# Optimization experiments

Measured on AMD Instinct MI355X. Metric: run time of the kernel, lower is better.

The kernel has to match this reference:

```python
import jax, jax.numpy as jnp
import numpy as np

K = 3
N_SENSOR = 10   # num_sensor N (forced by reshape(-1,10,10))
ADJ_N = 5       # adjacency size (forced by reshape(-1,5,5))
T_LEN = 4096    # seq_len
BATCH = 1024    # batch_size == num_of_filters (forced by output accumulation)


def _scaled_laplacian(W):
    # L_tilde = 2L/lambda_max - I, L = D - W (W symmetric -> eigvalsh valid)
    D = jnp.diag(jnp.sum(W, axis=1))
    L = D - W
    lam_max = jnp.max(jnp.linalg.eigvalsh(L))
    return (2.0 * L) / lam_max - jnp.eye(W.shape[0], dtype=W.dtype)


def _cheb_polynomials(L_tilde, K):
    polys = [jnp.eye(L_tilde.shape[0], dtype=L_tilde.dtype), L_tilde]
    for _ in range(2, K):
        polys.append(2.0 * (L_tilde @ polys[-1]) - polys[-2])
    return jnp.stack(polys[:K])  # (K, 5, 5)


def setup_inputs() -> dict:
    key = jax.random.key(0)
    kx, ka, ks, kt = jax.random.split(key, 4)
    x = jax.random.normal(kx, (T_LEN, BATCH, N_SENSOR), dtype=jnp.float32)
    W = jax.random.uniform(ka, (ADJ_N, ADJ_N), dtype=jnp.float32)
    # symmetric, zero-diagonal adjacency so the Laplacian is symmetric PSD-ish
    adj_mx = (W + W.T) * 0.5 * (1.0 - jnp.eye(ADJ_N, dtype=jnp.float32))
    spatial_attention = jax.random.uniform(ks, (BATCH, N_SENSOR, N_SENSOR), dtype=jnp.float32)
    Theta = jax.random.normal(kt, (K, N_SENSOR, BATCH), dtype=jnp.float32)  # (K, num_of_timesteps=10, num_of_filters=B)
    return {"x": x, "adj_mx": adj_mx, "spatial_attention": spatial_attention, "Theta": Theta}


def reference(x, adj_mx, spatial_attention, Theta):
    # adj path is detached in the torch code (cpu().detach().numpy())
    L_tilde = _scaled_laplacian(jax.lax.stop_gradient(adj_mx))
    cheb = _cheb_polynomials(L_tilde, K)                 # (K, 5, 5)
    T, B, N = x.shape                                    # (T, B, 10)
    x_t = jnp.swapaxes(x, 0, 2)                          # (10, B, T)
    sa = spatial_attention.reshape(-1, ADJ_N, ADJ_N)     # (4B, 5, 5)
    output = jnp.zeros((T, B, N), dtype=x.dtype)
    for k in range(K):
        T_k_with_at = (cheb[k] * sa).reshape(-1, N, N)   # (B, 10, 10)
        lhs = jnp.swapaxes(T_k_with_at, 0, 2)            # (10, 10, B)
        rhs = jnp.matmul(lhs, x_t)                       # (10, 10, B) @ (10, B, T) -> (10, 10, T)
        out_k = jnp.matmul(jnp.swapaxes(rhs, 1, 2), Theta[k])  # (10, T, 10) @ (10, B) -> (10, T, B)
        output = output + jnp.transpose(out_k, (1, 2, 0))       # (T, B, 10)
    return jax.nn.relu(output[..., None])                # (T, B, 10, 1)
```

## Files before the change

kernel.cpp:

```cpp
#include <hip/hip_runtime.h>
#include <math.h>

#define TLEN 4096
#define NB   1024
#define NS   10

typedef __attribute__((ext_vector_type(8))) short  s16x8;
typedef __attribute__((ext_vector_type(4))) float  f32x4;

__device__ void k0_body(const float* __restrict__ adj, float* __restrict__ ck) {
  float Wm[5][5], L[5][5];
  for (int r = 0; r < 5; ++r)
    for (int c = 0; c < 5; ++c) Wm[r][c] = adj[r*5+c];
  for (int r = 0; r < 5; ++r) {
    float d = 0.f;
    for (int c = 0; c < 5; ++c) d += Wm[r][c];
    for (int c = 0; c < 5; ++c) L[r][c] = (r==c ? d : 0.f) - Wm[r][c];
  }
  float v[5] = {0.7f, -1.1f, 0.9f, -0.8f, 1.3f};
  for (int it = 0; it < 96; ++it) {
    float w[5];
    for (int r = 0; r < 5; ++r) {
      float s = 0.f;
      for (int c = 0; c < 5; ++c) s += L[r][c]*v[c];
      w[r] = s;
    }
    float s = fabsf(w[0])+fabsf(w[1])+fabsf(w[2])+fabsf(w[3])+fabsf(w[4]);
    float inv = 1.f/s;
    for (int r = 0; r < 5; ++r) v[r] = w[r]*inv;
  }
  float num = 0.f, den = 0.f;
  for (int r = 0; r < 5; ++r) {
    float s = 0.f;
    for (int c = 0; c < 5; ++c) s += L[r][c]*v[c];
    num += v[r]*s; den += v[r]*v[r];
  }
  const float lam = num/den;
  float Lt[5][5];
  for (int r = 0; r < 5; ++r)
    for (int c = 0; c < 5; ++c)
      Lt[r][c] = 2.f*L[r][c]/lam - (r==c ? 1.f : 0.f);
  float T2[5][5];
  for (int r = 0; r < 5; ++r)
    for (int c = 0; c < 5; ++c) {
      float s = 0.f;
      for (int j = 0; j < 5; ++j) s += Lt[r][j]*Lt[j][c];
      T2[r][c] = 2.f*s - (r==c ? 1.f : 0.f);
    }
  for (int p = 0; p < 10; ++p)
    for (int n = 0; n < 10; ++n) {
      int m = (10*p+n) % 25, r = m/5, c = m%5;
      ck[0*100 + p*10+n] = (r==c ? 1.f : 0.f);
      ck[1*100 + p*10+n] = Lt[r][c];
      ck[2*100 + p*10+n] = T2[r][c];
    }
}

static __device__ __forceinline__ unsigned bfu(float f) {
  unsigned u = __float_as_uint(f);
  return (u + 0x7FFFu + ((u >> 16) & 1u)) >> 16;
}
static __device__ __forceinline__ unsigned pk2(float lo, float hi) {
  return bfu(lo) | (bfu(hi) << 16);
}

#define KC   128
#define NCHK 4
#define XB_U32 10240

__global__ __launch_bounds__(384) void ka_mfma(
    const float* __restrict__ x, const float* __restrict__ sa,
    const float* __restrict__ adj, float* __restrict__ ps,
    float* __restrict__ ck) {
  __shared__ __align__(16) unsigned lds[2*XB_U32];
  unsigned* XB = lds;
  unsigned* AS = lds + XB_U32;
  const int tid = threadIdx.x;
  if (tid >= 320) {
    if (tid == 320 && blockIdx.x == 0 && blockIdx.y == 0) k0_body(adj, ck);
    return;
  }
  const int w    = tid >> 6;
  const int l    = tid & 63;
  const int tl16 = l & 15;
  const int t0   = blockIdx.x * 16;
  const int b0   = blockIdx.y * 512;
  const int n0   = 2*w, n1 = 2*w + 1;

  const int xbp = tid / 5;
  const int xg  = (tid - xbp*5) * 2;
  const int xk  = 2*xbp;
  const int xks = xk >> 5, xkg = (xk & 31) >> 3, xj = xk & 7;
  const int xbase0 = ((xg*4 + xks)*64 + xkg*16)*4 + (xj >> 1);

  f32x4 acc0 = {0.f,0.f,0.f,0.f}, acc1 = {0.f,0.f,0.f,0.f};

  for (int c = 0; c < NCHK; ++c) {
    const int bc = b0 + c*KC;
    {
      const float* gp0 = x + (size_t)t0*(NB*NS) + (size_t)bc*NS + xbp*20 + xg;
      #pragma unroll
      for (int r = 0; r < 16; ++r) {
        const float* gp = gp0 + (size_t)r*(NB*NS);
        const float2 lo = *(const float2*)(gp);
        const float2 hi = *(const float2*)(gp + NS);
        const int base = xbase0 + r*4;
        XB[base]        = pk2(lo.x, hi.x);
        XB[base + 1024] = pk2(lo.y, hi.y);
      }
    }
    #pragma unroll
    for (int r = 0; r < 10; ++r) {
      const int s  = tid + 320*r;
      const int bp = s / 50;
      const int g  = (s - bp*50) * 2;
      const int p  = g / 10, n = g - p*10;
      const int k  = 2*bp;
      const float* gp = sa + (size_t)(bc + k)*100 + g;
      const float2 lo = *(const float2*)(gp);
      const float2 hi = *(const float2*)(gp + 100);
      const int ks = k >> 5, kg = (k & 31) >> 3, j = k & 7;
      const int base = ((n*4 + ks)*64 + kg*16 + p)*4 + (j >> 1);
      AS[base]        = pk2(lo.x, hi.x);
      AS[base + 1024] = pk2(lo.y, hi.y);
    }
    __syncthreads();
    const s16x8* XBf = (const s16x8*)XB;
    const s16x8* ASf = (const s16x8*)AS;
    #pragma unroll
    for (int ks = 0; ks < 4; ++ks) {
      const s16x8 a0 = ASf[(n0*4 + ks)*64 + l];
      const s16x8 bb0 = XBf[(n0*4 + ks)*64 + l];
      acc0 = __builtin_amdgcn_mfma_f32_16x16x32_bf16(a0, bb0, acc0, 0, 0, 0);
      const s16x8 a1 = ASf[(n1*4 + ks)*64 + l];
      const s16x8 bb1 = XBf[(n1*4 + ks)*64 + l];
      acc1 = __builtin_amdgcn_mfma_f32_16x16x32_bf16(a1, bb1, acc1, 0, 0, 0);
    }
    __syncthreads();
  }
  const int pg = (l >> 4) * 4;
  float* pd = ps + ((size_t)blockIdx.y*TLEN + t0 + tl16)*100;
  #pragma unroll
  for (int r = 0; r < 4; ++r) {
    const int p = pg + r;
    if (p < 10) {
      pd[n0*10 + p] = acc0[r];
      pd[n1*10 + p] = acc1[r];
    }
  }
}

#define TT 8
__global__ __launch_bounds__(256) void kc_out(const float* __restrict__ theta,
    const float* __restrict__ ck, const float* __restrict__ ps,
    float* __restrict__ out) {
  __shared__ __align__(16) float S[TT*120];
  __shared__ float C[300];
  __shared__ __align__(16) float stg[2][2560];
  const int tid = threadIdx.x;
  const int t0 = blockIdx.x * TT;
  const int b  = blockIdx.y * 256 + tid;
  for (int j = tid; j < 300; j += 256) C[j] = ck[j];
  for (int j = tid; j < TT*100; j += 256) {
    const int tt = j / 100, q = j - tt*100;
    float s = 0.f;
    #pragma unroll
    for (int sl = 0; sl < 2; ++sl)
      s += ps[((size_t)sl*TLEN + (t0+tt))*100 + q];
    S[tt*120 + (q/10)*12 + (q - (q/10)*10)] = s;
  }
  __syncthreads();
  float W[10][10];
  #pragma unroll
  for (int p = 0; p < 10; ++p) {
    const float th0 = theta[          p*NB + b];
    const float th1 = theta[10*NB  +  p*NB + b];
    const float th2 = theta[20*NB  +  p*NB + b];
    #pragma unroll
    for (int nn = 0; nn < 10; ++nn)
      W[p][nn] = C[p*10+nn]*th0 + C[100+p*10+nn]*th1 + C[200+p*10+nn]*th2;
  }
  for (int tt = 0; tt < TT; ++tt) {
    float acc[10];
    #pragma unroll
    for (int nn = 0; nn < 10; ++nn) {
      const float4 s0 = *(const float4*)(S + tt*120 + nn*12);
      const float4 s1 = *(const float4*)(S + tt*120 + nn*12 + 4);
      const float2 s2 = *(const float2*)(S + tt*120 + nn*12 + 8);
      acc[nn] = s0.x*W[0][nn] + s0.y*W[1][nn] + s0.z*W[2][nn] + s0.w*W[3][nn]
              + s1.x*W[4][nn] + s1.y*W[5][nn] + s1.z*W[6][nn] + s1.w*W[7][nn]
              + s2.x*W[8][nn] + s2.y*W[9][nn];
    }
    float* sg = stg[tt & 1];
    #pragma unroll
    for (int nn = 0; nn < 10; ++nn)
      sg[tid*10 + nn] = fmaxf(acc[nn], 0.f);
    __syncthreads();
    const float4* sp = (const float4*)sg;
    float4* op = (float4*)(out + (size_t)(t0+tt)*(NB*NS)
                               + (size_t)blockIdx.y*2560);
    op[tid]       = sp[tid];
    op[tid + 256] = sp[tid + 256];
    if (tid < 128) op[tid + 512] = sp[tid + 512];
  }
}

extern "C" void kernel_launch(void* const* d_in, const int* in_sizes, int n_in,
                              void* d_out, int out_size, void* d_ws, size_t ws_size,
                              hipStream_t stream) {
  const float* x   = (const float*)d_in[0];
  const float* adj = (const float*)d_in[1];
  const float* sa  = (const float*)d_in[2];
  const float* th  = (const float*)d_in[3];
  float* out = (float*)d_out;
  float* ws  = (float*)d_ws;
  float* ck  = ws;
  float* ps  = ws + 1024;
  hipLaunchKernelGGL(ka_mfma, dim3(TLEN/16, 2), dim3(384), 0, stream,
                     x, sa, adj, ps, ck);
  hipLaunchKernelGGL(kc_out,  dim3(TLEN/TT, NB/256), dim3(256), 0, stream,
                     th, ck, ps, out);
}
```

Before: 99.13 us.

## Double-buffer LDS staging in ka_mfma with register prefetch and swizzled layout

Restructures the first kernel's K loop into smaller 64-wide chunks with two LDS buffers. Global loads for the next chunk go into registers before the MFMAs on the current buffer, then are written to the other buffer, leaving one barrier per iteration. It also replaces the software bf16 rounding with the hardware v_cvt_pk_bf16_f32 instruction, adds an XOR swizzle to the LDS layout to reduce bank conflicts, and sets a 3-blocks-per-CU occupancy hint. The costs are more registers for the prefetch and a tighter register budget from the launch bound.

```diff
diff --git a/kernel.cpp b/kernel.cpp
--- a/kernel.cpp
+++ b/kernel.cpp
@@ -56,90 +56,122 @@
     }
 }
 
-static __device__ __forceinline__ unsigned bfu(float f) {
-  unsigned u = __float_as_uint(f);
-  return (u + 0x7FFFu + ((u >> 16) & 1u)) >> 16;
-}
-static __device__ __forceinline__ unsigned pk2(float lo, float hi) {
-  return bfu(lo) | (bfu(hi) << 16);
-}
-
-#define KC   128
-#define NCHK 4
-#define XB_U32 10240
-
-__global__ __launch_bounds__(384) void ka_mfma(
+static __device__ __forceinline__ unsigned cvtpk(float lo, float hi) {
+  unsigned r;
+  asm("v_cvt_pk_bf16_f32 %0, %1, %2" : "=v"(r) : "v"(lo), "v"(hi));
+  return r;
+}
+static __device__ __forceinline__ int swz(int P, int L) {
+  return P*64 + (L ^ ((P ^ (P >> 2)) & 7));
+}
+
+#define KC 64
+#define BUF_U32 10240
+
+__global__ __launch_bounds__(384, 3) void ka_mfma(
     const float* __restrict__ x, const float* __restrict__ sa,
     const float* __restrict__ adj, float* __restrict__ ps,
     float* __restrict__ ck) {
-  __shared__ __align__(16) unsigned lds[2*XB_U32];
-  unsigned* XB = lds;
-  unsigned* AS = lds + XB_U32;
+  __shared__ __align__(16) unsigned lds[2*BUF_U32];
   const int tid = threadIdx.x;
   if (tid >= 320) {
     if (tid == 320 && blockIdx.x == 0 && blockIdx.y == 0) k0_body(adj, ck);
     return;
   }
-  const int w    = tid >> 6;
-  const int l    = tid & 63;
-  const int tl16 = l & 15;
-  const int t0   = blockIdx.x * 16;
-  const int b0   = blockIdx.y * 512;
-  const int n0   = 2*w, n1 = 2*w + 1;
-
-  const int xbp = tid / 5;
-  const int xg  = (tid - xbp*5) * 2;
-  const int xk  = 2*xbp;
-  const int xks = xk >> 5, xkg = (xk & 31) >> 3, xj = xk & 7;
-  const int xbase0 = ((xg*4 + xks)*64 + xkg*16)*4 + (xj >> 1);
+  const int w  = tid >> 6;
+  const int l  = tid & 63;
+  const int t0 = blockIdx.x * 16;
+  const int b0 = blockIdx.y * 512;
+  const int n0 = 2*w, n1 = 2*w + 1;
+
+  const int bp = tid / 10;
+  const int rm = tid - bp*10;
+  const int q  = rm >> 1;
+  const int th = rm & 1;
+  const int gq = rm;
+  const int ksx = bp >> 4;
+  const int kgx = (bp & 15) >> 2;
+  const int jwx = bp & 3;
 
   f32x4 acc0 = {0.f,0.f,0.f,0.f}, acc1 = {0.f,0.f,0.f,0.f};
-
-  for (int c = 0; c < NCHK; ++c) {
-    const int bc = b0 + c*KC;
+  float2 xlo[8], xhi[8], slo[5], shi[5];
+
+  unsigned* cur = lds;
+  unsigned* nxt = lds + BUF_U32;
+
+  {
+    const float* xb = x + (size_t)(t0 + th*8)*(NB*NS) + (size_t)(b0 + 2*bp)*NS + 2*q;
+    #pragma unroll
+    for (int r = 0; r < 8; ++r) {
+      xlo[r] = *(const float2*)(xb + r*(NB*NS));
+      xhi[r] = *(const float2*)(xb + r*(NB*NS) + NS);
+    }
+    const float* sb = sa + (size_t)(b0 + 2*bp)*100 + gq*10;
+    #pragma unroll
+    for (int e = 0; e < 5; ++e) {
+      slo[e] = *(const float2*)(sb + 2*e);
+      shi[e] = *(const float2*)(sb + 100 + 2*e);
+    }
+  }
+  #pragma unroll
+  for (int r = 0; r < 8; ++r) {
+    const int L = kgx*16 + th*8 + r;
+    cur[swz((2*q  )*2 + ksx, L)*4 + jwx] = cvtpk(xlo[r].x, xhi[r].x);
+    cur[swz((2*q+1)*2 + ksx, L)*4 + jwx] = cvtpk(xlo[r].y, xhi[r].y);
+  }
+  #pragma unroll
+  for (int e = 0; e < 5; ++e) {
+    const int L = kgx*16 + gq;
+    cur[5120 + swz((2*e  )*2 + ksx, L)*4 + jwx] = cvtpk(slo[e].x, shi[e].x);
+    cur[5120 + swz((2*e+1)*2 + ksx, L)*4 + jwx] = cvtpk(slo[e].y, shi[e].y);
+  }
+
+  for (int c = 0; c < 8; ++c) {
+    __syncthreads();
+    if (c < 7) {
+      const int bc = b0 + (c+1)*KC;
+      const float* xb = x + (size_t)(t0 + th*8)*(NB*NS) + (size_t)(bc + 2*bp)*NS + 2*q;
+      #pragma unroll
+      for (int r = 0; r < 8; ++r) {
+        xlo[r] = *(const float2*)(xb + r*(NB*NS));
+        xhi[r] = *(const float2*)(xb + r*(NB*NS) + NS);
+      }
+      const float* sb = sa + (size_t)(bc + 2*bp)*100 + gq*10;
+      #pragma unroll
+      for (int e = 0; e < 5; ++e) {
+        slo[e] = *(const float2*)(sb + 2*e);
+        shi[e] = *(const float2*)(sb + 100 + 2*e);
+      }
+    }
     {
-      const float* gp0 = x + (size_t)t0*(NB*NS) + (size_t)bc*NS + xbp*20 + xg;
-      #pragma unroll
-      for (int r = 0; r < 16; ++r) {
-        const float* gp = gp0 + (size_t)r*(NB*NS);
-        const float2 lo = *(const float2*)(gp);
-        const float2 hi = *(const float2*)(gp + NS);
-        const int base = xbase0 + r*4;
-        XB[base]        = pk2(lo.x, hi.x);
-        XB[base + 1024] = pk2(lo.y, hi.y);
-      }
-    }
-    #pragma unroll
-    for (int r = 0; r < 10; ++r) {
-      const int s  = tid + 320*r;
-      const int bp = s / 50;
-      const int g  = (s - bp*50) * 2;
-      const int p  = g / 10, n = g - p*10;
-      const int k  = 2*bp;
-      const float* gp = sa + (size_t)(bc + k)*100 + g;
-      const float2 lo = *(const float2*)(gp);
-      const float2 hi = *(const float2*)(gp + 100);
-      const int ks = k >> 5, kg = (k & 31) >> 3, j = k & 7;
-      const int base = ((n*4 + ks)*64 + kg*16 + p)*4 + (j >> 1);
-      AS[base]        = pk2(lo.x, hi.x);
-      AS[base + 1024] = pk2(lo.y, hi.y);
-    }
-    __syncthreads();
-    const s16x8* XBf = (const s16x8*)XB;
-    const s16x8* ASf = (const s16x8*)AS;
-    #pragma unroll
-    for (int ks = 0; ks < 4; ++ks) {
-      const s16x8 a0 = ASf[(n0*4 + ks)*64 + l];
-      const s16x8 bb0 = XBf[(n0*4 + ks)*64 + l];
-      acc0 = __builtin_amdgcn_mfma_f32_16x16x32_bf16(a0, bb0, acc0, 0, 0, 0);
-      const s16x8 a1 = ASf[(n1*4 + ks)*64 + l];
-      const s16x8 bb1 = XBf[(n1*4 + ks)*64 + l];
-      acc1 = __builtin_amdgcn_mfma_f32_16x16x32_bf16(a1, bb1, acc1, 0, 0, 0);
-    }
-    __syncthreads();
+      const s16x8* XBf = (const s16x8*)cur;
+      const s16x8* ASf = (const s16x8*)(cur + 5120);
+      #pragma unroll
+      for (int ks = 0; ks < 2; ++ks) {
+        acc0 = __builtin_amdgcn_mfma_f32_16x16x32_bf16(
+                 ASf[swz(n0*2+ks, l)], XBf[swz(n0*2+ks, l)], acc0, 0, 0, 0);
+        acc1 = __builtin_amdgcn_mfma_f32_16x16x32_bf16(
+                 ASf[swz(n1*2+ks, l)], XBf[swz(n1*2+ks, l)], acc1, 0, 0, 0);
+      }
+    }
+    if (c < 7) {
+      #pragma unroll
+      for (int r = 0; r < 8; ++r) {
+        const int L = kgx*16 + th*8 + r;
+        nxt[swz((2*q  )*2 + ksx, L)*4 + jwx] = cvtpk(xlo[r].x, xhi[r].x);
+        nxt[swz((2*q+1)*2 + ksx, L)*4 + jwx] = cvtpk(xlo[r].y, xhi[r].y);
+      }
+      #pragma unroll
+      for (int e = 0; e < 5; ++e) {
+        const int L = kgx*16 + gq;
+        nxt[5120 + swz((2*e  )*2 + ksx, L)*4 + jwx] = cvtpk(slo[e].x, shi[e].x);
+        nxt[5120 + swz((2*e+1)*2 + ksx, L)*4 + jwx] = cvtpk(slo[e].y, shi[e].y);
+      }
+      unsigned* t = cur; cur = nxt; nxt = t;
+    }
   }
   const int pg = (l >> 4) * 4;
-  float* pd = ps + ((size_t)blockIdx.y*TLEN + t0 + tl16)*100;
+  float* pd = ps + ((size_t)blockIdx.y*TLEN + t0 + (l & 15))*100;
   #pragma unroll
   for (int r = 0; r < 4; ++r) {
     const int p = pg + r;
```

After: 98.50 us. No clear change (-0.6%).
